# Performance work log

Measured on AMD Instinct MI355X. Metric: run time of the kernel, lower is better.

Reference implementation:

```python
import jax, jax.numpy as jnp
import numpy as np

B, N, E, H = 8, 512, 1024, 128   # graphs, nodes, edges, hidden
T = 8                             # num_edge_types
HOPS = 3                          # graph_hops


def setup_inputs() -> dict:
    key = jax.random.key(0)
    ks = jax.random.split(key, 10)
    node_feature = jax.random.normal(ks[0], (B, N, H), dtype=jnp.float32)
    edge_vec = jax.random.randint(ks[1], (B, E), 0, T)  # per-edge type ids
    # sparse incidence matrices (one-hot edge endpoints), as the scipy .A densification does
    src = jax.random.randint(ks[2], (B, E), 0, N)
    tgt = jax.random.randint(ks[3], (B, E), 0, N)
    node2edge = jax.nn.one_hot(src, N, dtype=jnp.float32)                 # [B,E,N]
    edge2node = jnp.swapaxes(jax.nn.one_hot(tgt, N, dtype=jnp.float32), 1, 2)  # [B,N,E]
    s = 0.02  # xavier-ish init scale
    edge_weight_tensor = jax.random.normal(ks[4], (T, H * H), dtype=jnp.float32) * s
    Wz = jax.random.normal(ks[5], (2 * H, H), dtype=jnp.float32) * s
    Wr = jax.random.normal(ks[6], (2 * H, H), dtype=jnp.float32) * s
    Wt = jax.random.normal(ks[7], (2 * H, H), dtype=jnp.float32) * s
    Wf = jax.random.normal(ks[8], (4 * H, H), dtype=jnp.float32) * s
    bf = jnp.zeros((H,), dtype=jnp.float32)
    return {"node_feature": node_feature, "edge_vec": edge_vec,
            "node2edge": node2edge, "edge2node": edge2node,
            "edge_weight_tensor": edge_weight_tensor,
            "Wz": Wz, "Wr": Wr, "Wt": Wt, "Wf": Wf, "bf": bf}


def reference(node_feature, edge_vec, node2edge, edge2node,
              edge_weight_tensor, Wz, Wr, Wt, Wf, bf):
    Hd = node_feature.shape[-1]
    # gather per-edge weight matrices once (edge_vec is constant across hops)
    Wedge = edge_weight_tensor[edge_vec].reshape(edge_vec.shape + (Hd, Hd))  # [B,E,H,H]

    def mp(h, n2e, e2n):
        emb = jnp.einsum('ben,bnh->beh', n2e, h)          # gather node states to edges
        new = jnp.einsum('behd,bed->beh', Wedge, emb)     # per-edge-type matvec
        return jnp.einsum('bne,beh->bnh', e2n, new)       # scatter-aggregate to nodes

    def gru_step(h, a):
        x = jnp.concatenate([h, a], axis=-1)
        z = jax.nn.sigmoid(x @ Wz)
        r = jax.nn.sigmoid(x @ Wr)
        t = jnp.tanh(jnp.concatenate([r * h, a], axis=-1) @ Wt)
        return (1.0 - z) * h + z * t

    h = node_feature
    for _ in range(HOPS):
        bw = mp(h, node2edge, edge2node)
        fw = mp(h, jnp.swapaxes(edge2node, 1, 2), jnp.swapaxes(node2edge, 1, 2))
        # GatedFusion(fw, bw)
        z = jax.nn.sigmoid(jnp.concatenate([fw, bw, fw * bw, fw - bw], axis=-1) @ Wf + bf)
        agg = (1.0 - z) * fw + z * bw
        h = gru_step(h, agg)
    return h
```

## Files before the change

kernel.cpp:

```cpp
#include <hip/hip_runtime.h>

#define Bb 8
#define Nn 512
#define Ee 1024
#define Hh 128
#define Tt 8
#define FPAD 132

__device__ __forceinline__ float sigm(float x){ return 1.0f/(1.0f + __expf(-x)); }
__device__ __forceinline__ float tanh_fast(float x){ return 2.0f/(1.0f + __expf(-2.0f*x)) - 1.0f; }

__device__ __forceinline__ void fma4(float* acc, float4 x, float4 w0, float4 w1, float4 w2, float4 w3){
  acc[0] += x.x*w0.x + x.y*w1.x + x.z*w2.x + x.w*w3.x;
  acc[1] += x.x*w0.y + x.y*w1.y + x.z*w2.y + x.w*w3.y;
  acc[2] += x.x*w0.z + x.y*w1.z + x.z*w2.z + x.w*w3.z;
  acc[3] += x.x*w0.w + x.y*w1.w + x.z*w2.w + x.w*w3.w;
}

__global__ void k_extract(const float4* __restrict__ n2e, const float4* __restrict__ e2n,
                          int* __restrict__ src, int* __restrict__ tgt){
  const int total1 = Bb*Ee*Nn/4;
  for (int i = blockIdx.x*blockDim.x + threadIdx.x; i < total1; i += gridDim.x*blockDim.x){
    float4 v = n2e[i];
    if (v.x!=0.f || v.y!=0.f || v.z!=0.f || v.w!=0.f){
      int base = i*4;
      int row = base >> 9;
      int n   = base & 511;
      if (v.x!=0.f) src[row] = n;
      if (v.y!=0.f) src[row] = n+1;
      if (v.z!=0.f) src[row] = n+2;
      if (v.w!=0.f) src[row] = n+3;
    }
  }
  const int total2 = Bb*Nn*Ee/4;
  for (int i = blockIdx.x*blockDim.x + threadIdx.x; i < total2; i += gridDim.x*blockDim.x){
    float4 v = e2n[i];
    if (v.x!=0.f || v.y!=0.f || v.z!=0.f || v.w!=0.f){
      int base = i*4;
      int row = base >> 10;
      int e   = base & 1023;
      int b = row >> 9, n = row & 511;
      int* tp = tgt + b*Ee;
      if (v.x!=0.f) tp[e]   = n;
      if (v.y!=0.f) tp[e+1] = n;
      if (v.z!=0.f) tp[e+2] = n;
      if (v.w!=0.f) tp[e+3] = n;
    }
  }
}

__global__ void k_transW(const float* __restrict__ W, float* __restrict__ WT){
  int i = blockIdx.x*blockDim.x + threadIdx.x;
  if (i >= Tt*Hh*Hh) return;
  int t = i >> 14;
  int h = (i >> 7) & 127;
  int d = i & 127;
  WT[(t*Hh + d)*Hh + h] = W[i];
}

__global__ void k_prep(const float* __restrict__ Wf, float* __restrict__ Ff){
  int i = blockIdx.x*blockDim.x + threadIdx.x;
  if (i >= 384*Hh) return;
  int r = i >> 7, c = i & 127;
  float v;
  if (r < 128)      v = Wf[r*Hh + c] + Wf[(r+384)*Hh + c];
  else if (r < 256) v = Wf[r*Hh + c] - Wf[(r+256)*Hh + c];
  else              v = Wf[r*Hh + c];
  Ff[i] = v;
}

__global__ void k_sort(const int* __restrict__ ev, int* __restrict__ order, int* __restrict__ offs){
  __shared__ int cnt[Tt], offs_s[Tt+1], pos[Tt];
  int b = blockIdx.x, tid = threadIdx.x;
  if (tid < Tt) cnt[tid] = 0;
  __syncthreads();
  for (int e = tid; e < Ee; e += blockDim.x) atomicAdd(&cnt[ev[b*Ee+e]], 1);
  __syncthreads();
  if (tid == 0){ offs_s[0]=0; for (int t=0;t<Tt;t++) offs_s[t+1]=offs_s[t]+cnt[t]; }
  __syncthreads();
  if (tid < Tt) pos[tid] = offs_s[tid];
  if (tid < Tt+1) offs[b*(Tt+1)+tid] = offs_s[tid];
  __syncthreads();
  for (int e = tid; e < Ee; e += blockDim.x){
    int t = ev[b*Ee+e];
    int p = atomicAdd(&pos[t], 1);
    order[b*Ee + p] = e;
  }
}

__device__ __forceinline__ void ldw4(float4* b, const float* __restrict__ W, int k0){
  #pragma unroll
  for (int j = 0; j < 4; ++j) b[j] = *(const float4*)&W[(size_t)(k0+j)*Hh];
}

__global__ __launch_bounds__(256, 4) void k_edge_mp(
    const float* __restrict__ h, const float* __restrict__ WT,
    const int* __restrict__ order, const int* __restrict__ offs,
    const int* __restrict__ src, const int* __restrict__ tgt,
    float* __restrict__ bw, float* __restrict__ fw)
{
  int x = blockIdx.x;
  int dir = x & 1, bt = x >> 1, t = bt & 7, b = bt >> 3;
  int beg = offs[b*(Tt+1)+t], end = offs[b*(Tt+1)+t+1];
  int chunk0 = beg + blockIdx.y*32;
  if (chunk0 >= end) return;
  const int* gI = dir ? tgt : src;
  const int* sI = dir ? src : tgt;
  float* out = dir ? fw : bw;

  __shared__ int sGat[32];
  __shared__ int sSc[32];
  int tid = threadIdx.x, lane = tid & 63, w = tid >> 6;
  int e0 = (lane >> 3)*4;
  int c0 = w*32 + (lane & 7)*4;
  const float* __restrict__ Wg = WT + t*Hh*Hh + c0;
  const int rot = ((blockIdx.x + blockIdx.y) & 7) * 16;

  for (int chunk = chunk0; chunk < end; chunk += gridDim.y*32){
    int ne = min(32, end - chunk);
    __syncthreads();
    if (tid < 32){
      int ng = -1, ns = -1;
      if (tid < ne){
        int eid = order[b*Ee + chunk + tid];
        ng = gI[b*Ee + eid];
        ns = sI[b*Ee + eid];
      }
      sGat[tid] = ng; sSc[tid] = ns;
    }
    __syncthreads();

    const float* xr[4];
    int nsc[4];
    #pragma unroll
    for (int je = 0; je < 4; ++je){
      int ng = sGat[e0+je];
      xr[je] = h + (size_t)(b*Nn + (ng < 0 ? 0 : ng))*Hh;
      nsc[je] = sSc[e0+je];
    }

    float acc[4][4] = {};
    float4 wA[4], wB[4], xA[4], xB[4];
    int k0 = rot;
    ldw4(wA, Wg, k0);
    #pragma unroll
    for (int je = 0; je < 4; ++je) xA[je] = *(const float4*)&xr[je][k0];
    #pragma unroll 1
    for (int it = 0; it < 16; ++it){
      int k1 = (k0 + 4) & 127, k2 = (k0 + 8) & 127;
      ldw4(wB, Wg, k1);
      #pragma unroll
      for (int je = 0; je < 4; ++je) xB[je] = *(const float4*)&xr[je][k1];
      #pragma unroll
      for (int je = 0; je < 4; ++je) fma4(acc[je], xA[je], wA[0], wA[1], wA[2], wA[3]);
      ldw4(wA, Wg, k2);
      #pragma unroll
      for (int je = 0; je < 4; ++je) xA[je] = *(const float4*)&xr[je][k2];
      #pragma unroll
      for (int je = 0; je < 4; ++je) fma4(acc[je], xB[je], wB[0], wB[1], wB[2], wB[3]);
      k0 = k2;
    }

    #pragma unroll
    for (int j = 0; j < 4; ++j){
      int node = nsc[j];
      if (node >= 0){
        float* op = out + (size_t)(b*Nn + node)*Hh + c0;
        atomicAdd(op+0, acc[j][0]);
        atomicAdd(op+1, acc[j][1]);
        atomicAdd(op+2, acc[j][2]);
        atomicAdd(op+3, acc[j][3]);
      }
    }
  }
}


__device__ __forceinline__ void sec_row(const float* __restrict__ xrow,
                                        const float* __restrict__ Wg, int rot, float* acc){
  float4 wA[4], wB[4], xA, xB;
  int k0 = rot;
  ldw4(wA, Wg, k0);
  xA = *(const float4*)&xrow[k0];
  #pragma unroll 1
  for (int it = 0; it < 16; ++it){
    int k1 = (k0 + 4) & 127, k2 = (k0 + 8) & 127;
    ldw4(wB, Wg, k1);
    xB = *(const float4*)&xrow[k1];
    fma4(acc, xA, wA[0], wA[1], wA[2], wA[3]);
    ldw4(wA, Wg, k2);
    xA = *(const float4*)&xrow[k2];
    fma4(acc, xB, wB[0], wB[1], wB[2], wB[3]);
    k0 = k2;
  }
}

__device__ __forceinline__ void sec_prod(const float* __restrict__ a_, const float* __restrict__ b_,
                                         const float* __restrict__ Wg, int rot, float* acc){
  float4 wA[4], wB[4], xA, xB;
  int k0 = rot;
  ldw4(wA, Wg, k0);
  { float4 av = *(const float4*)&a_[k0], bv = *(const float4*)&b_[k0];
    xA = make_float4(av.x*bv.x, av.y*bv.y, av.z*bv.z, av.w*bv.w); }
  #pragma unroll 1
  for (int it = 0; it < 16; ++it){
    int k1 = (k0 + 4) & 127, k2 = (k0 + 8) & 127;
    ldw4(wB, Wg, k1);
    { float4 av = *(const float4*)&a_[k1], bv = *(const float4*)&b_[k1];
      xB = make_float4(av.x*bv.x, av.y*bv.y, av.z*bv.z, av.w*bv.w); }
    fma4(acc, xA, wA[0], wA[1], wA[2], wA[3]);
    ldw4(wA, Wg, k2);
    { float4 av = *(const float4*)&a_[k2], bv = *(const float4*)&b_[k2];
      xA = make_float4(av.x*bv.x, av.y*bv.y, av.z*bv.z, av.w*bv.w); }
    fma4(acc, xB, wB[0], wB[1], wB[2], wB[3]);
    k0 = k2;
  }
}

__device__ __forceinline__ void sec2(const float* __restrict__ xrow,
                                     const float* __restrict__ Wa, const float* __restrict__ Wc,
                                     int rot, float* acc1, float* acc2){
  float4 aA[4], aB[4], cA[4], cB[4], xA, xB;
  int k0 = rot;
  ldw4(aA, Wa, k0); ldw4(cA, Wc, k0);
  xA = *(const float4*)&xrow[k0];
  #pragma unroll 1
  for (int it = 0; it < 16; ++it){
    int k1 = (k0 + 4) & 127, k2 = (k0 + 8) & 127;
    ldw4(aB, Wa, k1); ldw4(cB, Wc, k1);
    xB = *(const float4*)&xrow[k1];
    fma4(acc1, xA, aA[0], aA[1], aA[2], aA[3]);
    fma4(acc2, xA, cA[0], cA[1], cA[2], cA[3]);
    ldw4(aA, Wa, k2); ldw4(cA, Wc, k2);
    xA = *(const float4*)&xrow[k2];
    fma4(acc1, xB, aB[0], aB[1], aB[2], aB[3]);
    fma4(acc2, xB, cB[0], cB[1], cB[2], cB[3]);
    k0 = k2;
  }
}

__global__ __launch_bounds__(256, 4) void k_fuse_gru(
    const float* __restrict__ hin, const float* __restrict__ fw, const float* __restrict__ bw,
    const float* __restrict__ Ff, const float* __restrict__ bfv,
    const float* __restrict__ Wz, const float* __restrict__ Wr, const float* __restrict__ Wt,
    float* __restrict__ hout, float* __restrict__ zf, float* __restrict__ zb)
{
  __shared__ float sA[8][FPAD];
  __shared__ float sR[8][FPAD];
  int tid  = threadIdx.x;
  int row0 = blockIdx.x * 8;
  int lane = tid & 63, w = tid >> 6;
  int r    = lane >> 3;
  int c0   = w*32 + (lane & 7)*4;
  const int rot = (blockIdx.x & 7) * 16;

  const float* __restrict__ frow = fw  + (size_t)(row0 + r)*Hh;
  const float* __restrict__ brow = bw  + (size_t)(row0 + r)*Hh;
  const float* __restrict__ hrow = hin + (size_t)(row0 + r)*Hh;
  float4 bias = *(const float4*)&bfv[c0];

  float af[4] = {0,0,0,0};
  sec_row (frow, Ff + c0,              rot, af);
  sec_row (brow, Ff + 128*Hh + c0,     rot, af);
  sec_prod(frow, brow, Ff + 256*Hh + c0, rot, af);

  {
    float4 fv = *(const float4*)&frow[c0];
    float4 bv = *(const float4*)&brow[c0];
    float bb[4] = {bias.x, bias.y, bias.z, bias.w};
    float fvv[4] = {fv.x, fv.y, fv.z, fv.w};
    float bvv[4] = {bv.x, bv.y, bv.z, bv.w};
    float ag[4];
    #pragma unroll
    for (int j = 0; j < 4; ++j){
      float z = sigm(af[j] + bb[j]);
      ag[j] = (1.0f - z)*fvv[j] + z*bvv[j];
    }
    *(float4*)&sA[r][c0] = make_float4(ag[0], ag[1], ag[2], ag[3]);
  }

  float az[4] = {0,0,0,0}, ar[4] = {0,0,0,0};
  sec2(hrow, Wz + c0, Wr + c0, rot, az, ar);
  __syncthreads();
  sec2(&sA[r][0], Wz + 128*Hh + c0, Wr + 128*Hh + c0, rot, az, ar);

  float zz[4], hv[4];
  {
    float4 hv4 = *(const float4*)&hrow[c0];
    hv[0]=hv4.x; hv[1]=hv4.y; hv[2]=hv4.z; hv[3]=hv4.w;
    float rh[4];
    #pragma unroll
    for (int j = 0; j < 4; ++j){
      zz[j] = sigm(az[j]);
      rh[j] = sigm(ar[j]) * hv[j];
    }
    *(float4*)&sR[r][c0] = make_float4(rh[0], rh[1], rh[2], rh[3]);
  }

  float at[4] = {0,0,0,0};
  sec_row(&sA[r][0], Wt + 128*Hh + c0, rot, at);
  __syncthreads();
  sec_row(&sR[r][0], Wt + c0, rot, at);

  float o[4];
  #pragma unroll
  for (int j = 0; j < 4; ++j){
    float t = tanh_fast(at[j]);
    o[j] = (1.0f - zz[j])*hv[j] + zz[j]*t;
  }
  *(float4*)&hout[(size_t)(row0 + r)*Hh + c0] = make_float4(o[0], o[1], o[2], o[3]);

  {
    int ir = tid >> 5, k0 = (tid & 31)*4;
    size_t g = (size_t)(row0 + ir)*Hh + k0;
    float4 zv = {0.f,0.f,0.f,0.f};
    *(float4*)&zf[g] = zv;
    *(float4*)&zb[g] = zv;
  }
}

extern "C" void kernel_launch(void* const* d_in, const int* in_sizes, int n_in,
                              void* d_out, int out_size, void* d_ws, size_t ws_size,
                              hipStream_t stream){
  const float* node_feature = (const float*)d_in[0];
  const int*   edge_vec     = (const int*)d_in[1];
  const float* n2e          = (const float*)d_in[2];
  const float* e2n          = (const float*)d_in[3];
  const float* Wtensor      = (const float*)d_in[4];
  const float* Wz           = (const float*)d_in[5];
  const float* Wr           = (const float*)d_in[6];
  const float* Wt           = (const float*)d_in[7];
  const float* Wf           = (const float*)d_in[8];
  const float* bf           = (const float*)d_in[9];
  float* out = (float*)d_out;

  char* p = (char*)d_ws;
  int* src   = (int*)p; p += Bb*Ee*4;
  int* tgt   = (int*)p; p += Bb*Ee*4;
  int* order = (int*)p; p += Bb*Ee*4;
  int* offs  = (int*)p; p += 4096;
  float* WT  = (float*)p; p += (size_t)Tt*Hh*Hh*4;
  float* Ff  = (float*)p; p += (size_t)384*Hh*4;
  float* bwp = (float*)p; p += (size_t)Bb*Nn*Hh*4;
  float* fwp = (float*)p; p += (size_t)Bb*Nn*Hh*4;
  float* h1  = (float*)p; p += (size_t)Bb*Nn*Hh*4;

  k_extract<<<1024, 256, 0, stream>>>((const float4*)n2e, (const float4*)e2n, src, tgt);
  k_transW<<<(Tt*Hh*Hh + 255)/256, 256, 0, stream>>>(Wtensor, WT);
  k_prep<<<(384*Hh + 255)/256, 256, 0, stream>>>(Wf, Ff);
  k_sort<<<Bb, 256, 0, stream>>>(edge_vec, order, offs);
  hipMemsetAsync(bwp, 0, (size_t)2*Bb*Nn*Hh*4, stream);

  const float* hin = node_feature;
  float* houts[3] = { out, h1, out };
  for (int hop = 0; hop < 3; ++hop){
    k_edge_mp<<<dim3(Bb*Tt*2, 4), 256, 0, stream>>>(hin, WT, order, offs, src, tgt, bwp, fwp);
    k_fuse_gru<<<(Bb*Nn)/8, 256, 0, stream>>>(hin, fwp, bwp, Ff, bf, Wz, Wr, Wt, houts[hop], fwp, bwp);
    hin = houts[hop];
  }
}
```

Measured before the change: 499.4 us.

## Split K across half-waves in fuse_gru and halve edge chunk per block

The fused gate/GRU kernel now handles 4 rows per block instead of 8. Each half-wave computes half of the K dimension, and the two partial sums are combined with a cross-lane shuffle, which doubles the block count and shortens the dependent FMA chains. The edge message-passing kernel processes 16 edges per chunk with a grid.y of 8, doubling parallelism there too. The manual double-buffered rotated-K loops are replaced with simple unrolled loops. In exchange, each row block reads the weight matrices more times, and the removed K rotation may increase same-address contention.

```diff
diff --git a/kernel.cpp b/kernel.cpp
--- a/kernel.cpp
+++ b/kernel.cpp
@@ -88,9 +88,54 @@
   }
 }
 
-__device__ __forceinline__ void ldw4(float4* b, const float* __restrict__ W, int k0){
-  #pragma unroll
-  for (int j = 0; j < 4; ++j) b[j] = *(const float4*)&W[(size_t)(k0+j)*Hh];
+__device__ __forceinline__ void sec64(const float* __restrict__ x, const float* __restrict__ Wg,
+                                      int ko, float* acc){
+  #pragma unroll 4
+  for (int k = 0; k < 64; k += 4){
+    int kk = ko + k;
+    float4 xv = *(const float4*)&x[kk];
+    float4 w0 = *(const float4*)&Wg[(size_t)(kk+0)*Hh];
+    float4 w1 = *(const float4*)&Wg[(size_t)(kk+1)*Hh];
+    float4 w2 = *(const float4*)&Wg[(size_t)(kk+2)*Hh];
+    float4 w3 = *(const float4*)&Wg[(size_t)(kk+3)*Hh];
+    fma4(acc, xv, w0, w1, w2, w3);
+  }
+}
+
+__device__ __forceinline__ void prod64(const float* __restrict__ a_, const float* __restrict__ b_,
+                                       const float* __restrict__ Wg, int ko, float* acc){
+  #pragma unroll 4
+  for (int k = 0; k < 64; k += 4){
+    int kk = ko + k;
+    float4 av = *(const float4*)&a_[kk];
+    float4 bv = *(const float4*)&b_[kk];
+    float4 xv = make_float4(av.x*bv.x, av.y*bv.y, av.z*bv.z, av.w*bv.w);
+    float4 w0 = *(const float4*)&Wg[(size_t)(kk+0)*Hh];
+    float4 w1 = *(const float4*)&Wg[(size_t)(kk+1)*Hh];
+    float4 w2 = *(const float4*)&Wg[(size_t)(kk+2)*Hh];
+    float4 w3 = *(const float4*)&Wg[(size_t)(kk+3)*Hh];
+    fma4(acc, xv, w0, w1, w2, w3);
+  }
+}
+
+__device__ __forceinline__ void sec2_64(const float* __restrict__ x,
+                                        const float* __restrict__ Wa, const float* __restrict__ Wc,
+                                        int ko, float* acc1, float* acc2){
+  #pragma unroll 2
+  for (int k = 0; k < 64; k += 4){
+    int kk = ko + k;
+    float4 xv = *(const float4*)&x[kk];
+    float4 a0 = *(const float4*)&Wa[(size_t)(kk+0)*Hh];
+    float4 a1 = *(const float4*)&Wa[(size_t)(kk+1)*Hh];
+    float4 a2 = *(const float4*)&Wa[(size_t)(kk+2)*Hh];
+    float4 a3 = *(const float4*)&Wa[(size_t)(kk+3)*Hh];
+    fma4(acc1, xv, a0, a1, a2, a3);
+    float4 c0_ = *(const float4*)&Wc[(size_t)(kk+0)*Hh];
+    float4 c1_ = *(const float4*)&Wc[(size_t)(kk+1)*Hh];
+    float4 c2_ = *(const float4*)&Wc[(size_t)(kk+2)*Hh];
+    float4 c3_ = *(const float4*)&Wc[(size_t)(kk+3)*Hh];
+    fma4(acc2, xv, c0_, c1_, c2_, c3_);
+  }
 }
 
 __global__ __launch_bounds__(256, 4) void k_edge_mp(
@@ -102,24 +147,23 @@
   int x = blockIdx.x;
   int dir = x & 1, bt = x >> 1, t = bt & 7, b = bt >> 3;
   int beg = offs[b*(Tt+1)+t], end = offs[b*(Tt+1)+t+1];
-  int chunk0 = beg + blockIdx.y*32;
+  int chunk0 = beg + blockIdx.y*16;
   if (chunk0 >= end) return;
   const int* gI = dir ? tgt : src;
   const int* sI = dir ? src : tgt;
   float* out = dir ? fw : bw;
 
-  __shared__ int sGat[32];
-  __shared__ int sSc[32];
+  __shared__ int sGat[16];
+  __shared__ int sSc[16];
   int tid = threadIdx.x, lane = tid & 63, w = tid >> 6;
-  int e0 = (lane >> 3)*4;
+  int e0 = (lane >> 3)*2;
   int c0 = w*32 + (lane & 7)*4;
   const float* __restrict__ Wg = WT + t*Hh*Hh + c0;
-  const int rot = ((blockIdx.x + blockIdx.y) & 7) * 16;
-
-  for (int chunk = chunk0; chunk < end; chunk += gridDim.y*32){
-    int ne = min(32, end - chunk);
+
+  for (int chunk = chunk0; chunk < end; chunk += gridDim.y*16){
+    int ne = min(16, end - chunk);
     __syncthreads();
-    if (tid < 32){
+    if (tid < 16){
       int ng = -1, ns = -1;
       if (tid < ne){
         int eid = order[b*Ee + chunk + tid];
@@ -130,39 +174,30 @@
     }
     __syncthreads();
 
-    const float* xr[4];
-    int nsc[4];
+    const float* xr[2];
+    int nsc[2];
     #pragma unroll
-    for (int je = 0; je < 4; ++je){
+    for (int je = 0; je < 2; ++je){
       int ng = sGat[e0+je];
       xr[je] = h + (size_t)(b*Nn + (ng < 0 ? 0 : ng))*Hh;
       nsc[je] = sSc[e0+je];
     }
 
-    float acc[4][4] = {};
-    float4 wA[4], wB[4], xA[4], xB[4];
-    int k0 = rot;
-    ldw4(wA, Wg, k0);
+    float acc[2][4] = {};
+    #pragma unroll 4
+    for (int k = 0; k < Hh; k += 4){
+      float4 w0 = *(const float4*)&Wg[(size_t)(k+0)*Hh];
+      float4 w1 = *(const float4*)&Wg[(size_t)(k+1)*Hh];
+      float4 w2 = *(const float4*)&Wg[(size_t)(k+2)*Hh];
+      float4 w3 = *(const float4*)&Wg[(size_t)(k+3)*Hh];
+      float4 x0 = *(const float4*)&xr[0][k];
+      float4 x1 = *(const float4*)&xr[1][k];
+      fma4(acc[0], x0, w0, w1, w2, w3);
+      fma4(acc[1], x1, w0, w1, w2, w3);
+    }
+
     #pragma unroll
-    for (int je = 0; je < 4; ++je) xA[je] = *(const float4*)&xr[je][k0];
-    #pragma unroll 1
-    for (int it = 0; it < 16; ++it){
-      int k1 = (k0 + 4) & 127, k2 = (k0 + 8) & 127;
-      ldw4(wB, Wg, k1);
-      #pragma unroll
-      for (int je = 0; je < 4; ++je) xB[je] = *(const float4*)&xr[je][k1];
-      #pragma unroll
-      for (int je = 0; je < 4; ++je) fma4(acc[je], xA[je], wA[0], wA[1], wA[2], wA[3]);
-      ldw4(wA, Wg, k2);
-      #pragma unroll
-      for (int je = 0; je < 4; ++je) xA[je] = *(const float4*)&xr[je][k2];
-      #pragma unroll
-      for (int je = 0; je < 4; ++je) fma4(acc[je], xB[je], wB[0], wB[1], wB[2], wB[3]);
-      k0 = k2;
-    }
-
-    #pragma unroll
-    for (int j = 0; j < 4; ++j){
+    for (int j = 0; j < 2; ++j){
       int node = nsc[j];
       if (node >= 0){
         float* op = out + (size_t)(b*Nn + node)*Hh + c0;
@@ -175,84 +210,22 @@
   }
 }
 
-
-__device__ __forceinline__ void sec_row(const float* __restrict__ xrow,
-                                        const float* __restrict__ Wg, int rot, float* acc){
-  float4 wA[4], wB[4], xA, xB;
-  int k0 = rot;
-  ldw4(wA, Wg, k0);
-  xA = *(const float4*)&xrow[k0];
-  #pragma unroll 1
-  for (int it = 0; it < 16; ++it){
-    int k1 = (k0 + 4) & 127, k2 = (k0 + 8) & 127;
-    ldw4(wB, Wg, k1);
-    xB = *(const float4*)&xrow[k1];
-    fma4(acc, xA, wA[0], wA[1], wA[2], wA[3]);
-    ldw4(wA, Wg, k2);
-    xA = *(const float4*)&xrow[k2];
-    fma4(acc, xB, wB[0], wB[1], wB[2], wB[3]);
-    k0 = k2;
-  }
-}
-
-__device__ __forceinline__ void sec_prod(const float* __restrict__ a_, const float* __restrict__ b_,
-                                         const float* __restrict__ Wg, int rot, float* acc){
-  float4 wA[4], wB[4], xA, xB;
-  int k0 = rot;
-  ldw4(wA, Wg, k0);
-  { float4 av = *(const float4*)&a_[k0], bv = *(const float4*)&b_[k0];
-    xA = make_float4(av.x*bv.x, av.y*bv.y, av.z*bv.z, av.w*bv.w); }
-  #pragma unroll 1
-  for (int it = 0; it < 16; ++it){
-    int k1 = (k0 + 4) & 127, k2 = (k0 + 8) & 127;
-    ldw4(wB, Wg, k1);
-    { float4 av = *(const float4*)&a_[k1], bv = *(const float4*)&b_[k1];
-      xB = make_float4(av.x*bv.x, av.y*bv.y, av.z*bv.z, av.w*bv.w); }
-    fma4(acc, xA, wA[0], wA[1], wA[2], wA[3]);
-    ldw4(wA, Wg, k2);
-    { float4 av = *(const float4*)&a_[k2], bv = *(const float4*)&b_[k2];
-      xA = make_float4(av.x*bv.x, av.y*bv.y, av.z*bv.z, av.w*bv.w); }
-    fma4(acc, xB, wB[0], wB[1], wB[2], wB[3]);
-    k0 = k2;
-  }
-}
-
-__device__ __forceinline__ void sec2(const float* __restrict__ xrow,
-                                     const float* __restrict__ Wa, const float* __restrict__ Wc,
-                                     int rot, float* acc1, float* acc2){
-  float4 aA[4], aB[4], cA[4], cB[4], xA, xB;
-  int k0 = rot;
-  ldw4(aA, Wa, k0); ldw4(cA, Wc, k0);
-  xA = *(const float4*)&xrow[k0];
-  #pragma unroll 1
-  for (int it = 0; it < 16; ++it){
-    int k1 = (k0 + 4) & 127, k2 = (k0 + 8) & 127;
-    ldw4(aB, Wa, k1); ldw4(cB, Wc, k1);
-    xB = *(const float4*)&xrow[k1];
-    fma4(acc1, xA, aA[0], aA[1], aA[2], aA[3]);
-    fma4(acc2, xA, cA[0], cA[1], cA[2], cA[3]);
-    ldw4(aA, Wa, k2); ldw4(cA, Wc, k2);
-    xA = *(const float4*)&xrow[k2];
-    fma4(acc1, xB, aB[0], aB[1], aB[2], aB[3]);
-    fma4(acc2, xB, cB[0], cB[1], cB[2], cB[3]);
-    k0 = k2;
-  }
-}
-
 __global__ __launch_bounds__(256, 4) void k_fuse_gru(
     const float* __restrict__ hin, const float* __restrict__ fw, const float* __restrict__ bw,
     const float* __restrict__ Ff, const float* __restrict__ bfv,
     const float* __restrict__ Wz, const float* __restrict__ Wr, const float* __restrict__ Wt,
     float* __restrict__ hout, float* __restrict__ zf, float* __restrict__ zb)
 {
-  __shared__ float sA[8][FPAD];
-  __shared__ float sR[8][FPAD];
+  __shared__ float sA[4][FPAD];
+  __shared__ float sR[4][FPAD];
   int tid  = threadIdx.x;
-  int row0 = blockIdx.x * 8;
+  int row0 = blockIdx.x * 4;
   int lane = tid & 63, w = tid >> 6;
-  int r    = lane >> 3;
-  int c0   = w*32 + (lane & 7)*4;
-  const int rot = (blockIdx.x & 7) * 16;
+  int kh   = lane >> 5;
+  int l5   = lane & 31;
+  int r    = l5 >> 3;
+  int c0   = w*32 + (l5 & 7)*4;
+  int ko   = kh*64;
 
   const float* __restrict__ frow = fw  + (size_t)(row0 + r)*Hh;
   const float* __restrict__ brow = bw  + (size_t)(row0 + r)*Hh;
@@ -260,14 +233,16 @@
   float4 bias = *(const float4*)&bfv[c0];
 
   float af[4] = {0,0,0,0};
-  sec_row (frow, Ff + c0,              rot, af);
-  sec_row (brow, Ff + 128*Hh + c0,     rot, af);
-  sec_prod(frow, brow, Ff + 256*Hh + c0, rot, af);
+  sec64 (frow, Ff + c0,              ko, af);
+  sec64 (brow, Ff + 128*Hh + c0,     ko, af);
+  prod64(frow, brow, Ff + 256*Hh + c0, ko, af);
+  #pragma unroll
+  for (int j = 0; j < 4; ++j) af[j] += __shfl_xor(af[j], 32);
 
   {
     float4 fv = *(const float4*)&frow[c0];
     float4 bv = *(const float4*)&brow[c0];
-    float bb[4] = {bias.x, bias.y, bias.z, bias.w};
+    float bb[4]  = {bias.x, bias.y, bias.z, bias.w};
     float fvv[4] = {fv.x, fv.y, fv.z, fv.w};
     float bvv[4] = {bv.x, bv.y, bv.z, bv.w};
     float ag[4];
@@ -280,9 +255,14 @@
   }
 
   float az[4] = {0,0,0,0}, ar[4] = {0,0,0,0};
-  sec2(hrow, Wz + c0, Wr + c0, rot, az, ar);
-  __syncthreads();
-  sec2(&sA[r][0], Wz + 128*Hh + c0, Wr + 128*Hh + c0, rot, az, ar);
+  sec2_64(hrow, Wz + c0, Wr + c0, ko, az, ar);
+  __syncthreads();
+  sec2_64(&sA[r][0], Wz + 128*Hh + c0, Wr + 128*Hh + c0, ko, az, ar);
+  #pragma unroll
+  for (int j = 0; j < 4; ++j){
+    az[j] += __shfl_xor(az[j], 32);
+    ar[j] += __shfl_xor(ar[j], 32);
+  }
 
   float zz[4], hv[4];
   {
@@ -298,9 +278,11 @@
   }
 
   float at[4] = {0,0,0,0};
-  sec_row(&sA[r][0], Wt + 128*Hh + c0, rot, at);
-  __syncthreads();
-  sec_row(&sR[r][0], Wt + c0, rot, at);
+  sec64(&sA[r][0], Wt + 128*Hh + c0, ko, at);
+  __syncthreads();
+  sec64(&sR[r][0], Wt + c0, ko, at);
+  #pragma unroll
+  for (int j = 0; j < 4; ++j) at[j] += __shfl_xor(at[j], 32);
 
   float o[4];
   #pragma unroll
@@ -311,11 +293,11 @@
   *(float4*)&hout[(size_t)(row0 + r)*Hh + c0] = make_float4(o[0], o[1], o[2], o[3]);
 
   {
-    int ir = tid >> 5, k0 = (tid & 31)*4;
+    int ir = tid >> 6, k0 = (tid & 63)*2;
     size_t g = (size_t)(row0 + ir)*Hh + k0;
-    float4 zv = {0.f,0.f,0.f,0.f};
-    *(float4*)&zf[g] = zv;
-    *(float4*)&zb[g] = zv;
+    float2 zv = {0.f, 0.f};
+    *(float2*)&zf[g] = zv;
+    *(float2*)&zb[g] = zv;
   }
 }
 
@@ -354,8 +336,8 @@
   const float* hin = node_feature;
   float* houts[3] = { out, h1, out };
   for (int hop = 0; hop < 3; ++hop){
-    k_edge_mp<<<dim3(Bb*Tt*2, 4), 256, 0, stream>>>(hin, WT, order, offs, src, tgt, bwp, fwp);
-    k_fuse_gru<<<(Bb*Nn)/8, 256, 0, stream>>>(hin, fwp, bwp, Ff, bf, Wz, Wr, Wt, houts[hop], fwp, bwp);
+    k_edge_mp<<<dim3(Bb*Tt*2, 8), 256, 0, stream>>>(hin, WT, order, offs, src, tgt, bwp, fwp);
+    k_fuse_gru<<<(Bb*Nn)/4, 256, 0, stream>>>(hin, fwp, bwp, Ff, bf, Wz, Wr, Wt, houts[hop], fwp, bwp);
     hin = houts[hop];
   }
 }
```

After: 498.5 us. About the same (-0.2%).
